# Optimization experiments

Measured on AMD Instinct MI355X. Metric: run time of the kernel, lower is better.

The kernel has to match this reference:

```python
import jax, jax.numpy as jnp
import numpy as np

NUM_STATES = 8
HIDDEN_DIM = 1024
BATCH = 16384
DT = 0.01
PLANCK = 1.0
EPS_NORM = 1e-8
EPS_LOG = 1e-12


def setup_inputs() -> dict:
    key = jax.random.key(0)
    k1, k2, k3, k4, k5 = jax.random.split(key, 5)
    inv_sqrt_d = 1.0 / np.sqrt(HIDDEN_DIM)
    return {
        "input_state": jax.random.normal(k1, (BATCH, HIDDEN_DIM), dtype=jnp.float32),
        "amplitude_real": jax.random.normal(k2, (NUM_STATES, HIDDEN_DIM), dtype=jnp.float32) * inv_sqrt_d,
        "amplitude_imag": jax.random.normal(k3, (NUM_STATES, HIDDEN_DIM), dtype=jnp.float32) * inv_sqrt_d,
        "hamiltonian": jax.random.normal(k4, (NUM_STATES, NUM_STATES), dtype=jnp.float32) * 0.01,
        "projections": jax.random.normal(k5, (NUM_STATES, HIDDEN_DIM, HIDDEN_DIM), dtype=jnp.float32) * 0.01,
    }


def reference(input_state, amplitude_real, amplitude_imag, hamiltonian, projections):
    # complex amplitudes, normalized per state over hidden dim
    amps = amplitude_real + 1j * amplitude_imag  # [S, D] complex64
    norms = jnp.sum(jnp.abs(amps) ** 2, axis=1, keepdims=True)
    amps = amps / jnp.sqrt(norms + EPS_NORM)

    # unitary Hamiltonian evolution: expm(-i H dt / hbar) on the tiny SxS matrix
    H = (hamiltonian + hamiltonian.T) * 0.5
    U = jax.scipy.linalg.expm((-1j * DT / PLANCK) * H.astype(jnp.complex64))  # [S, S]
    amps = U @ amps  # [S, D]

    # decoherence at time_step=0: factor exp(0)=1, thermal noise scale 0 -> identity

    # superposed output: out[b,e] = sum_s Re(amps[s,e]) * (x @ P_s)[b,e]
    w = jnp.real(amps)  # [S, D]
    proj = jnp.einsum('bd,sde->bse', input_state, projections)  # [B, S, D]
    measured_output = jnp.einsum('bse,se->be', proj, w)  # [B, D]

    # measurement probabilities (computational basis)
    probs = jnp.abs(amps) ** 2
    probs = probs / (probs.sum(axis=0, keepdims=True) + EPS_NORM)
    collapse_prob = probs.mean(axis=1)  # [S]

    # metrics on rank-1 density matrix rho = outer(v, conj(v)), v = amps.flatten():
    # eigenvalues are {||v||^2, 0, ...} so the von Neumann entropy reduces to one term,
    # and sum|rho| = (sum|v|)^2, tr|diag| = sum|v|^2.
    v_abs = jnp.abs(amps.reshape(-1))
    lam = jnp.sum(v_abs ** 2)
    entanglement_entropy = -(lam * jnp.log(lam + EPS_LOG))
    coherence = jnp.sum(v_abs) ** 2 - lam

    amplitude_distribution = jnp.abs(amps) ** 2
    phase_evolution = jnp.angle(amps)

    return (measured_output, collapse_prob, entanglement_entropy, coherence,
            amplitude_distribution, phase_evolution)
```

## Files before the change

### kernel.cpp

```cpp
#include <hip/hip_runtime.h>
#include <hip/hip_bf16.h>

#define NSTATES 8
#define HD      1024
#define NBATCH  16384
#define NT      16

#define OUT_MEAS 0
#define OUT_CP   16777216
#define OUT_ENT  16777224
#define OUT_COH  16777225
#define OUT_AD   16777226
#define OUT_PH   16785418

typedef __attribute__((ext_vector_type(8))) short short8;
typedef __attribute__((ext_vector_type(4))) float f32x4;

__device__ __forceinline__ short f2bf(float f) {
    union { float f; unsigned u; } x; x.f = f;
    unsigned r = x.u + 0x7fffu + ((x.u >> 16) & 1u);
    return (short)(r >> 16);
}

__device__ __forceinline__ short8 pack8(float4 a, float4 b) {
    short8 v;
    v[0] = f2bf(a.x); v[1] = f2bf(a.y); v[2] = f2bf(a.z); v[3] = f2bf(a.w);
    v[4] = f2bf(b.x); v[5] = f2bf(b.y); v[6] = f2bf(b.z); v[7] = f2bf(b.w);
    return v;
}

__global__ __launch_bounds__(1024) void k_amps(const float* __restrict__ AR,
                                               const float* __restrict__ AI,
                                               const float* __restrict__ H,
                                               float* __restrict__ out,
                                               float* __restrict__ w) {
    __shared__ float redA[16 * NSTATES];
    __shared__ float redB[16 * 10];
    __shared__ float norms[NSTATES];
    __shared__ float sA[8][8], sA2[8][8], sA3[8][8];
    __shared__ float Ur[8][8], Ui[8][8];
    __shared__ float lamsa[2];

    const int tid = threadIdx.x;
    const int lane = tid & 63, wid = tid >> 6;
    const int d = tid;

    float arv[NSTATES], aiv[NSTATES];
    #pragma unroll
    for (int s = 0; s < NSTATES; s++) {
        arv[s] = AR[s * HD + d];
        aiv[s] = AI[s * HD + d];
    }
    float p[NSTATES];
    #pragma unroll
    for (int s = 0; s < NSTATES; s++) p[s] = arv[s] * arv[s] + aiv[s] * aiv[s];
    #pragma unroll
    for (int s = 0; s < NSTATES; s++)
        #pragma unroll
        for (int o = 32; o > 0; o >>= 1) p[s] += __shfl_down(p[s], o, 64);
    if (lane == 0)
        #pragma unroll
        for (int s = 0; s < NSTATES; s++) redA[wid * NSTATES + s] = p[s];
    if (tid < 64) {
        int i = tid >> 3, j = tid & 7;
        sA[i][j] = 0.5f * (H[i * 8 + j] + H[j * 8 + i]) * 0.01f;
    }
    __syncthreads();
    if (tid < 8) {
        float acc = 0.f;
        #pragma unroll
        for (int v = 0; v < 16; v++) acc += redA[v * NSTATES + tid];
        norms[tid] = acc;
    }
    if (tid < 64) {
        int i = tid >> 3, j = tid & 7;
        float acc = 0.f;
        #pragma unroll
        for (int k = 0; k < 8; k++) acc += sA[i][k] * sA[k][j];
        sA2[i][j] = acc;
    }
    __syncthreads();
    if (tid < 64) {
        int i = tid >> 3, j = tid & 7;
        float acc = 0.f;
        #pragma unroll
        for (int k = 0; k < 8; k++) acc += sA2[i][k] * sA[k][j];
        sA3[i][j] = acc;
        Ur[i][j] = ((i == j) ? 1.f : 0.f) - 0.5f * sA2[i][j];
        Ui[i][j] = -(sA[i][j] - sA3[i][j] * (1.f / 6.f));
    }
    __syncthreads();

    #pragma unroll
    for (int s = 0; s < NSTATES; s++) {
        float inv = 1.0f / sqrtf(norms[s] + 1e-8f);
        arv[s] *= inv;
        aiv[s] *= inv;
    }
    float nr[NSTATES], ni[NSTATES];
    #pragma unroll
    for (int s = 0; s < NSTATES; s++) {
        float xr = 0.f, xi = 0.f;
        #pragma unroll
        for (int t = 0; t < NSTATES; t++) {
            float ur = Ur[s][t], ui = Ui[s][t];
            xr += ur * arv[t] - ui * aiv[t];
            xi += ur * aiv[t] + ui * arv[t];
        }
        nr[s] = xr; ni[s] = xi;
    }
    float dist[NSTATES], csum = 0.f, sabs = 0.f;
    #pragma unroll
    for (int s = 0; s < NSTATES; s++) {
        dist[s] = nr[s] * nr[s] + ni[s] * ni[s];
        csum += dist[s];
        sabs += sqrtf(dist[s]);
    }
    #pragma unroll
    for (int s = 0; s < NSTATES; s++) {
        out[OUT_AD + s * HD + d] = dist[s];
        out[OUT_PH + s * HD + d] = atan2f(ni[s], nr[s]);
        w[s * HD + d] = nr[s];
    }
    float cinv = 1.0f / (csum + 1e-8f);
    float q[10];
    #pragma unroll
    for (int s = 0; s < NSTATES; s++) q[s] = dist[s] * cinv;
    q[8] = csum; q[9] = sabs;
    #pragma unroll
    for (int v = 0; v < 10; v++)
        #pragma unroll
        for (int o = 32; o > 0; o >>= 1) q[v] += __shfl_down(q[v], o, 64);
    if (lane == 0)
        #pragma unroll
        for (int v = 0; v < 10; v++) redB[wid * 10 + v] = q[v];
    __syncthreads();
    if (tid < 10) {
        float acc = 0.f;
        #pragma unroll
        for (int v = 0; v < 16; v++) acc += redB[v * 10 + tid];
        if (tid < 8)       out[OUT_CP + tid] = acc * (1.0f / HD);
        else               lamsa[tid - 8] = acc;
    }
    __syncthreads();
    if (tid == 0) {
        float lam = lamsa[0], sa = lamsa[1];
        out[OUT_ENT] = -(lam * logf(lam + 1e-12f));
        out[OUT_COH] = sa * sa - lam;
    }
}

__global__ __launch_bounds__(256) void k_project_t(const float* __restrict__ P,
                                                   const float* __restrict__ w,
                                                   short* __restrict__ Mt) {
    __shared__ float tile[64][65];
    int d0 = (blockIdx.x >> 4) * 64;
    int e0 = (blockIdx.x & 15) * 64;
    int tx = threadIdx.x & 63, ty = threadIdx.x >> 6;
    float wv[NSTATES];
    #pragma unroll
    for (int s = 0; s < NSTATES; s++) wv[s] = w[s * HD + e0 + tx];
    #pragma unroll
    for (int j = 0; j < 16; j++) {
        int r = ty + 4 * j;
        float acc = 0.f;
        #pragma unroll
        for (int s = 0; s < NSTATES; s++)
            acc += wv[s] * P[(size_t)s * HD * HD + (size_t)(d0 + r) * HD + e0 + tx];
        tile[r][tx] = acc;
    }
    __syncthreads();
    #pragma unroll
    for (int j = 0; j < 16; j++) {
        int er = ty + 4 * j;
        Mt[(size_t)(e0 + er) * HD + d0 + tx] = f2bf(tile[tx][er]);
    }
}


__device__ __forceinline__ void stage_half_B(const short* __restrict__ srcBase,
                                             int rowbase, int h, int t2,
                                             short* dst, const int* goff,
                                             const int* ldsoff) {
    #pragma unroll
    for (int i = 0; i < 2; i++) {
        const short* g = srcBase + (size_t)(rowbase + h * 128) * HD + t2 * 64 + goff[i];
        __builtin_amdgcn_global_load_lds(
            (const __attribute__((address_space(1))) void*)g,
            (__attribute__((address_space(3))) void*)(dst + h * 8192 + ldsoff[i]),
            16, 0, 0);
    }
}

#define XLOAD(h, t2)                                                           \
    {                                                                          \
        const float* base_ = X + (size_t)(brow + (h) * 128) * HD + (t2) * 64;  \
        xr[0] = *reinterpret_cast<const float4*>(base_ + goff[0]);             \
        xr[1] = *reinterpret_cast<const float4*>(base_ + goff[0] + 4);         \
        xr[2] = *reinterpret_cast<const float4*>(base_ + goff[1]);             \
        xr[3] = *reinterpret_cast<const float4*>(base_ + goff[1] + 4);         \
    }

#define XWRITE(dst, h)                                                         \
    {                                                                          \
        *reinterpret_cast<short8*>((dst) + (h) * 8192 + ldsoff[0]) = pack8(xr[0], xr[1]); \
        *reinterpret_cast<short8*>((dst) + (h) * 8192 + ldsoff[1]) = pack8(xr[2], xr[3]); \
    }

#define LOAD_A(qa)                                                             \
    _Pragma("unroll") for (int mf = 0; mf < 4; mf++)                           \
    _Pragma("unroll") for (int kk = 0; kk < 2; kk++)                           \
        af[mf][kk] = *reinterpret_cast<const short8*>(                         \
            &Acur[((qa) * 128 + wr64 + mf * 16 + ln15) * 64 + kx[kk]]);

#define LOAD_B(qb)                                                             \
    _Pragma("unroll") for (int nf = 0; nf < 2; nf++)                           \
    _Pragma("unroll") for (int kk = 0; kk < 2; kk++)                           \
        bf[nf][kk] = *reinterpret_cast<const short8*>(                         \
            &Bcur[((qb) * 128 + wn32 + nf * 16 + ln15) * 64 + kx[kk]]);

#define MFMA_P(qa, qb)                                                         \
    _Pragma("unroll") for (int mf = 0; mf < 4; mf++)                           \
    _Pragma("unroll") for (int nf = 0; nf < 2; nf++)                           \
    _Pragma("unroll") for (int kk = 0; kk < 2; kk++)                           \
        acc[(qa) * 4 + mf][(qb) * 2 + nf] =                                    \
            __builtin_amdgcn_mfma_f32_16x16x32_bf16(                           \
                af[mf][kk], bf[nf][kk], acc[(qa) * 4 + mf][(qb) * 2 + nf], 0, 0, 0);

#define PHASE_MID()                                                            \
    __builtin_amdgcn_s_barrier();                                              \
    __builtin_amdgcn_s_setprio(1);

#define PHASE_END()                                                            \
    __builtin_amdgcn_s_setprio(0);                                             \
    __builtin_amdgcn_s_barrier();

__global__ __launch_bounds__(512, 1) void k_gemm_8p(const float* __restrict__ X,
                                                    const short* __restrict__ Mt,
                                                    float* __restrict__ out) {
    __shared__ short As[2][256 * 64];
    __shared__ short Bs[2][256 * 64];

    const int bid = blockIdx.x;
    const int swz = (bid & 7) * 32 + (bid >> 3);
    const int brow = (swz >> 2) * 256;
    const int bcol = (swz & 3) * 256;

    const int tid  = threadIdx.x;
    const int lane = tid & 63, wid = tid >> 6;
    const int wr = wid >> 2, wn = wid & 3;
    const int ln15 = lane & 15, l16 = lane >> 4;
    const int wr64 = wr * 64;
    const int wn32 = wn * 32;

    int kx[2];
    kx[0] = ((l16 + 0) ^ (ln15 & 7)) * 8;
    kx[1] = ((l16 + 4) ^ (ln15 & 7)) * 8;

    int goff[2], ldsoff[2];
    #pragma unroll
    for (int i = 0; i < 2; i++) {
        int c = tid + 512 * i;
        int row = c >> 3, kc = c & 7;
        goff[i]   = row * HD + ((kc ^ (row & 7)) * 8);
        ldsoff[i] = c * 8;
    }

    short* A0 = &As[0][0]; short* A1b = &As[1][0];
    short* B0 = &Bs[0][0]; short* B1b = &Bs[1][0];

    f32x4 acc[8][4];
    #pragma unroll
    for (int m = 0; m < 8; m++)
        #pragma unroll
        for (int n = 0; n < 4; n++) acc[m][n] = (f32x4){0.f, 0.f, 0.f, 0.f};

    float4 xr[4];

    XLOAD(0, 0);
    float4 xr2[4];
    {
        const float* base_ = X + (size_t)(brow + 128) * HD;
        xr2[0] = *reinterpret_cast<const float4*>(base_ + goff[0]);
        xr2[1] = *reinterpret_cast<const float4*>(base_ + goff[0] + 4);
        xr2[2] = *reinterpret_cast<const float4*>(base_ + goff[1]);
        xr2[3] = *reinterpret_cast<const float4*>(base_ + goff[1] + 4);
    }
    stage_half_B(Mt, bcol, 0, 0, B0, goff, ldsoff);
    stage_half_B(Mt, bcol, 1, 0, B0, goff, ldsoff);
    stage_half_B(Mt, bcol, 1, 1, B1b, goff, ldsoff);
    XWRITE(A0, 0);
    *reinterpret_cast<short8*>(A0 + 8192 + ldsoff[0]) = pack8(xr2[0], xr2[1]);
    *reinterpret_cast<short8*>(A0 + 8192 + ldsoff[1]) = pack8(xr2[2], xr2[3]);
    asm volatile("s_waitcnt vmcnt(2) lgkmcnt(0)" ::: "memory");
    __builtin_amdgcn_s_barrier();

    short8 af[4][2], bf[2][2];

    #pragma unroll 1
    for (int t = 0; t < NT; t++) {
        const int cur = t & 1;
        short* Acur  = cur ? A1b : A0;
        short* Bcur  = cur ? B1b : B0;
        short* Anext = cur ? A0 : A1b;
        short* Bnext = cur ? B0 : B1b;

        LOAD_A(0); LOAD_B(0);
        if (t + 1 < NT) XLOAD(0, (t + 1));
        PHASE_MID();
        MFMA_P(0, 0);
        PHASE_END();

        LOAD_B(1);
        if (t + 1 < NT) {
            stage_half_B(Mt, bcol, 0, t + 1, Bnext, goff, ldsoff);
            XWRITE(Anext, 0);
        }
        PHASE_MID();
        MFMA_P(0, 1);
        __builtin_amdgcn_s_setprio(0);
        asm volatile("s_waitcnt lgkmcnt(0)" ::: "memory");
        __builtin_amdgcn_s_barrier();

        LOAD_A(1);
        if (t + 1 < NT) XLOAD(1, (t + 1));
        PHASE_MID();
        MFMA_P(1, 1);
        PHASE_END();

        LOAD_B(0);
        if (t + 1 < NT) XWRITE(Anext, 1);
        if (t + 2 < NT) stage_half_B(Mt, bcol, 1, t + 2, Bcur, goff, ldsoff);
        PHASE_MID();
        MFMA_P(1, 0);
        __builtin_amdgcn_s_setprio(0);
        if (t + 2 < NT) asm volatile("s_waitcnt vmcnt(2) lgkmcnt(0)" ::: "memory");
        else            asm volatile("s_waitcnt vmcnt(0) lgkmcnt(0)" ::: "memory");
        __builtin_amdgcn_s_barrier();
    }

    #pragma unroll
    for (int qa = 0; qa < 2; qa++)
        #pragma unroll
        for (int mf = 0; mf < 4; mf++)
            #pragma unroll
            for (int qb = 0; qb < 2; qb++)
                #pragma unroll
                for (int nf = 0; nf < 2; nf++)
                    #pragma unroll
                    for (int j = 0; j < 4; j++) {
                        int r = brow + qa * 128 + wr64 + mf * 16 + l16 * 4 + j;
                        int c = bcol + qb * 128 + wn32 + nf * 16 + ln15;
                        out[(size_t)r * HD + c] = acc[qa * 4 + mf][qb * 2 + nf][j];
                    }
}

extern "C" void kernel_launch(void* const* d_in, const int* in_sizes, int n_in,
                              void* d_out, int out_size, void* d_ws, size_t ws_size,
                              hipStream_t stream) {
    const float* X  = (const float*)d_in[0];
    const float* AR = (const float*)d_in[1];
    const float* AI = (const float*)d_in[2];
    const float* H  = (const float*)d_in[3];
    const float* P  = (const float*)d_in[4];
    float* out = (float*)d_out;

    char* ws = (char*)d_ws;
    float* w  = (float*)ws;
    short* Mt = (short*)(ws + 32768);

    k_amps<<<1, 1024, 0, stream>>>(AR, AI, H, out, w);
    k_project_t<<<256, 256, 0, stream>>>(P, w, Mt);
    k_gemm_8p<<<(NBATCH / 256) * (HD / 256), 512, 0, stream>>>(X, Mt, out);
}
```

Baseline: 76.43 us.

## Single-buffer A tile in LDS and prefetch X one phase earlier

The bf16 A tile (converted from fp32 X) now lives in a single LDS buffer instead of a double buffer. Each half is overwritten only after all waves have pulled their fragments into registers. The global X loads are issued a full phase earlier, so the fp32 data sits in registers across an MFMA phase before being packed and written. The vmcnt wait thresholds are adjusted to match. The goal is to cut LDS footprint and hide X load latency better, at the risk of implicit waits on xr registers and tighter ordering hazards on the shared A buffer.

```diff
diff --git a/kernel.cpp b/kernel.cpp
--- a/kernel.cpp
+++ b/kernel.cpp
@@ -192,26 +192,26 @@
     }
 }
 
-#define XLOAD(h, t2)                                                           \
+#define XLOAD_TO(dst, h, t2)                                                   \
     {                                                                          \
         const float* base_ = X + (size_t)(brow + (h) * 128) * HD + (t2) * 64;  \
-        xr[0] = *reinterpret_cast<const float4*>(base_ + goff[0]);             \
-        xr[1] = *reinterpret_cast<const float4*>(base_ + goff[0] + 4);         \
-        xr[2] = *reinterpret_cast<const float4*>(base_ + goff[1]);             \
-        xr[3] = *reinterpret_cast<const float4*>(base_ + goff[1] + 4);         \
-    }
-
-#define XWRITE(dst, h)                                                         \
+        dst[0] = *reinterpret_cast<const float4*>(base_ + goff[0]);            \
+        dst[1] = *reinterpret_cast<const float4*>(base_ + goff[0] + 4);        \
+        dst[2] = *reinterpret_cast<const float4*>(base_ + goff[1]);            \
+        dst[3] = *reinterpret_cast<const float4*>(base_ + goff[1] + 4);        \
+    }
+
+#define XWRITE_FROM(src, h)                                                    \
     {                                                                          \
-        *reinterpret_cast<short8*>((dst) + (h) * 8192 + ldsoff[0]) = pack8(xr[0], xr[1]); \
-        *reinterpret_cast<short8*>((dst) + (h) * 8192 + ldsoff[1]) = pack8(xr[2], xr[3]); \
+        *reinterpret_cast<short8*>(As + (h) * 8192 + ldsoff[0]) = pack8(src[0], src[1]); \
+        *reinterpret_cast<short8*>(As + (h) * 8192 + ldsoff[1]) = pack8(src[2], src[3]); \
     }
 
 #define LOAD_A(qa)                                                             \
     _Pragma("unroll") for (int mf = 0; mf < 4; mf++)                           \
     _Pragma("unroll") for (int kk = 0; kk < 2; kk++)                           \
         af[mf][kk] = *reinterpret_cast<const short8*>(                         \
-            &Acur[((qa) * 128 + wr64 + mf * 16 + ln15) * 64 + kx[kk]]);
+            &As[((qa) * 128 + wr64 + mf * 16 + ln15) * 64 + kx[kk]]);
 
 #define LOAD_B(qb)                                                             \
     _Pragma("unroll") for (int nf = 0; nf < 2; nf++)                           \
@@ -238,7 +238,7 @@
 __global__ __launch_bounds__(512, 1) void k_gemm_8p(const float* __restrict__ X,
                                                     const short* __restrict__ Mt,
                                                     float* __restrict__ out) {
-    __shared__ short As[2][256 * 64];
+    __shared__ short As[256 * 64];
     __shared__ short Bs[2][256 * 64];
 
     const int bid = blockIdx.x;
@@ -266,8 +266,7 @@
         ldsoff[i] = c * 8;
     }
 
-    short* A0 = &As[0][0]; short* A1b = &As[1][0];
-    short* B0 = &Bs[0][0]; short* B1b = &Bs[1][0];
+    short* B0 = &Bs[0][0]; short* B1 = &Bs[1][0];
 
     f32x4 acc[8][4];
     #pragma unroll
@@ -277,44 +276,37 @@
 
     float4 xr[4];
 
-    XLOAD(0, 0);
-    float4 xr2[4];
     {
-        const float* base_ = X + (size_t)(brow + 128) * HD;
-        xr2[0] = *reinterpret_cast<const float4*>(base_ + goff[0]);
-        xr2[1] = *reinterpret_cast<const float4*>(base_ + goff[0] + 4);
-        xr2[2] = *reinterpret_cast<const float4*>(base_ + goff[1]);
-        xr2[3] = *reinterpret_cast<const float4*>(base_ + goff[1] + 4);
-    }
-    stage_half_B(Mt, bcol, 0, 0, B0, goff, ldsoff);
-    stage_half_B(Mt, bcol, 1, 0, B0, goff, ldsoff);
-    stage_half_B(Mt, bcol, 1, 1, B1b, goff, ldsoff);
-    XWRITE(A0, 0);
-    *reinterpret_cast<short8*>(A0 + 8192 + ldsoff[0]) = pack8(xr2[0], xr2[1]);
-    *reinterpret_cast<short8*>(A0 + 8192 + ldsoff[1]) = pack8(xr2[2], xr2[3]);
-    asm volatile("s_waitcnt vmcnt(2) lgkmcnt(0)" ::: "memory");
+        float4 t0[4], t1[4];
+        XLOAD_TO(t0, 0, 0);
+        XLOAD_TO(t1, 1, 0);
+        stage_half_B(Mt, bcol, 0, 0, B0, goff, ldsoff);
+        stage_half_B(Mt, bcol, 1, 0, B0, goff, ldsoff);
+        XWRITE_FROM(t0, 0);
+        XWRITE_FROM(t1, 1);
+        stage_half_B(Mt, bcol, 1, 1, B1, goff, ldsoff);
+        XLOAD_TO(xr, 0, 1);
+    }
+    asm volatile("s_waitcnt vmcnt(6) lgkmcnt(0)" ::: "memory");
     __builtin_amdgcn_s_barrier();
 
     short8 af[4][2], bf[2][2];
 
     #pragma unroll 1
     for (int t = 0; t < NT; t++) {
-        const int cur = t & 1;
-        short* Acur  = cur ? A1b : A0;
-        short* Bcur  = cur ? B1b : B0;
-        short* Anext = cur ? A0 : A1b;
-        short* Bnext = cur ? B0 : B1b;
+        short* Bcur  = (t & 1) ? B1 : B0;
+        short* Bnext = (t & 1) ? B0 : B1;
 
         LOAD_A(0); LOAD_B(0);
-        if (t + 1 < NT) XLOAD(0, (t + 1));
         PHASE_MID();
         MFMA_P(0, 0);
         PHASE_END();
 
         LOAD_B(1);
         if (t + 1 < NT) {
+            XWRITE_FROM(xr, 0);
+            XLOAD_TO(xr, 1, (t + 1));
             stage_half_B(Mt, bcol, 0, t + 1, Bnext, goff, ldsoff);
-            XWRITE(Anext, 0);
         }
         PHASE_MID();
         MFMA_P(0, 1);
@@ -323,19 +315,21 @@
         __builtin_amdgcn_s_barrier();
 
         LOAD_A(1);
-        if (t + 1 < NT) XLOAD(1, (t + 1));
         PHASE_MID();
         MFMA_P(1, 1);
         PHASE_END();
 
         LOAD_B(0);
-        if (t + 1 < NT) XWRITE(Anext, 1);
-        if (t + 2 < NT) stage_half_B(Mt, bcol, 1, t + 2, Bcur, goff, ldsoff);
+        if (t + 1 < NT) XWRITE_FROM(xr, 1);
+        if (t + 2 < NT) {
+            XLOAD_TO(xr, 0, (t + 2));
+            stage_half_B(Mt, bcol, 1, t + 2, Bcur, goff, ldsoff);
+        }
         PHASE_MID();
         MFMA_P(1, 0);
         __builtin_amdgcn_s_setprio(0);
-        if (t + 2 < NT) asm volatile("s_waitcnt vmcnt(2) lgkmcnt(0)" ::: "memory");
-        else            asm volatile("s_waitcnt vmcnt(0) lgkmcnt(0)" ::: "memory");
+        if (t + 2 < NT)      asm volatile("s_waitcnt vmcnt(6) lgkmcnt(0)" ::: "memory");
+        else if (t + 1 < NT) asm volatile("s_waitcnt vmcnt(0) lgkmcnt(0)" ::: "memory");
         __builtin_amdgcn_s_barrier();
     }
 
```

After: 73.98 us. 1.03x faster.
